# Performance work log

Measured on AMD Instinct MI355X. Metric: run time of the kernel, lower is better.

Reference implementation:

```python
import jax, jax.numpy as jnp
import numpy as np
import math

N_HEAD = 16
K_SPARSE = 64

def setup_inputs() -> dict:
    key = jax.random.key(0)
    ks = jax.random.split(key, 12)
    B, T, C = 1, 2048, 1024
    s = 0.02
    return {
        "x":   jax.random.normal(ks[0], (B, T, C), jnp.float32),
        "Wq":  jax.random.normal(ks[1], (C, C), jnp.float32) * s,
        "bq":  jax.random.normal(ks[2], (C,), jnp.float32) * s,
        "Wk":  jax.random.normal(ks[3], (C, C), jnp.float32) * s,
        "bk":  jax.random.normal(ks[4], (C,), jnp.float32) * s,
        "Wv":  jax.random.normal(ks[5], (C, C), jnp.float32) * s,
        "bv":  jax.random.normal(ks[6], (C,), jnp.float32) * s,
        "Wo":  jax.random.normal(ks[7], (C, C), jnp.float32) * s,
        "bo":  jax.random.normal(ks[8], (C,), jnp.float32) * s,
        "Wks": jax.random.normal(ks[9], (C,), jnp.float32) * s,
        "bks": jax.random.normal(ks[10], (), jnp.float32) * s,
    }

def reference(x, Wq, bq, Wk, bk, Wv, bv, Wo, bo, Wks, bks):
    B, T, C = x.shape
    nh = N_HEAD
    hs = C // nh
    k_val = min(K_SPARSE, T)

    # projections -> (B, nh, T, hs)   (torch Linear: x @ W.T + b)
    q = (x @ Wq.T + bq).reshape(B, T, nh, hs).transpose(0, 2, 1, 3)
    k = (x @ Wk.T + bk).reshape(B, T, nh, hs).transpose(0, 2, 1, 3)
    v = (x @ Wv.T + bv).reshape(B, T, nh, hs).transpose(0, 2, 1, 3)

    # key scorer: per-token scalar score (B, T)
    key_scores = x @ Wks + bks

    # causal masking of scores, then per-query top-k key selection
    pos = jnp.arange(T)
    causal = pos[None, :] <= pos[:, None]                      # (T, T), True where key<=query
    masked = jnp.where(causal[None], key_scores[:, None, :], -jnp.inf)  # (B, T, T)
    _, top_k_idx = jax.lax.top_k(masked, k_val)                # (B, T, k)
    top_k_idx = jnp.minimum(top_k_idx, pos[None, :, None])     # clamp to <= query pos

    # gather sparse keys/values: (B, nh, T, k, hs)
    bi = jnp.arange(B)[:, None, None, None]
    hi = jnp.arange(nh)[None, :, None, None]
    gi = top_k_idx[:, None, :, :]                              # (B, 1, T, k)
    sparse_k = k[bi, hi, gi]                                   # (B, nh, T, k, hs)
    sparse_v = v[bi, hi, gi]

    scale = 1.0 / math.sqrt(hs)
    logits = jnp.einsum('bhtd,bhtkd->bhtk', q, sparse_k) * scale
    probs = jax.nn.softmax(logits, axis=-1)
    out = jnp.einsum('bhtk,bhtkd->bhtd', probs, sparse_v)      # (B, nh, T, hs)
    out = out.transpose(0, 2, 1, 3).reshape(B, T, C)
    return out @ Wo.T + bo
```

## Files before the change

kernel.cpp:

```cpp
#include <hip/hip_runtime.h>
#include <hip/hip_bf16.h>
#include <cstdint>
#include <cstddef>

#define T_DIM 2048
#define C_DIM 1024
#define NH 16
#define HS 64
#define KSP 64

#define GBM 128
#define GBN 64
#define GBK 64
#define GPAD 72

typedef short short8 __attribute__((ext_vector_type(8)));
typedef float f32x4 __attribute__((ext_vector_type(4)));

__device__ __forceinline__ float bfu2f(unsigned short u) {
  unsigned v = ((unsigned)u) << 16;
  return __builtin_bit_cast(float, v);
}
__device__ __forceinline__ unsigned short f2bfu(float f) {
  unsigned u = __builtin_bit_cast(unsigned, f);
  unsigned r = (u + 0x7fffu + ((u >> 16) & 1u)) >> 16;
  return (unsigned short)r;
}
__device__ __forceinline__ float bflo(unsigned u) {
  return __builtin_bit_cast(float, u << 16);
}
__device__ __forceinline__ float bfhi(unsigned u) {
  return __builtin_bit_cast(float, u & 0xffff0000u);
}

__global__ __launch_bounds__(256) void convert_all_kernel(
    const float* __restrict__ x, const float* __restrict__ Wq,
    const float* __restrict__ Wk, const float* __restrict__ Wv,
    const float* __restrict__ Wo,
    unsigned short* __restrict__ xb, unsigned short* __restrict__ Wqb,
    unsigned short* __restrict__ Wkb, unsigned short* __restrict__ Wvb,
    unsigned short* __restrict__ Wob) {
  const int i = blockIdx.x * 256 + threadIdx.x;
  const int NX4 = T_DIM * C_DIM / 4;
  const int NW4 = C_DIM * C_DIM / 4;
  const float* src;
  unsigned short* dst;
  int j = i;
  if (j < NX4) { src = x; dst = xb; }
  else {
    j -= NX4;
    int w = j / NW4;
    j -= w * NW4;
    src = (w == 0) ? Wq : (w == 1) ? Wk : (w == 2) ? Wv : Wo;
    dst = (w == 0) ? Wqb : (w == 1) ? Wkb : (w == 2) ? Wvb : Wob;
  }
  float4 f = reinterpret_cast<const float4*>(src)[j];
  ushort4 o;
  o.x = f2bfu(f.x); o.y = f2bfu(f.y); o.z = f2bfu(f.z); o.w = f2bfu(f.w);
  reinterpret_cast<ushort4*>(dst)[j] = o;
}

__global__ __launch_bounds__(256) void scores_kernel(
    const float* __restrict__ x, const float* __restrict__ Wks,
    const float* __restrict__ bks, float* __restrict__ scores) {
  const int t = blockIdx.x * 4 + (threadIdx.x >> 6);
  const int lane = threadIdx.x & 63;
  const float* xrow = x + (size_t)t * C_DIM;
  float acc = 0.f;
  #pragma unroll 4
  for (int i = lane; i < C_DIM; i += 64)
    acc += xrow[i] * Wks[i];
  #pragma unroll
  for (int o = 32; o; o >>= 1) acc += __shfl_xor(acc, o);
  if (lane == 0) scores[t] = acc + bks[0];
}

__global__ __launch_bounds__(256) void rank_sort_kernel(
    const float* __restrict__ scores, int* __restrict__ sorted_idx) {
  __shared__ float ss[T_DIM];
  const int tid = threadIdx.x;
  for (int j = tid; j < T_DIM; j += 256) ss[j] = scores[j];
  __syncthreads();
  const int w = tid >> 6, lane = tid & 63;
  const int i = blockIdx.x * 4 + w;
  const float si = ss[i];
  int rank = 0;
  #pragma unroll
  for (int step = 0; step < T_DIM / 64; ++step) {
    const int j = step * 64 + lane;
    const float sj = ss[j];
    rank += (int)((sj > si) || (sj == si && j < i));
  }
  #pragma unroll
  for (int o = 32; o; o >>= 1) rank += __shfl_xor(rank, o);
  if (lane == 0) sorted_idx[rank] = i;
}

__global__ __launch_bounds__(256) void select_topk_kernel(
    const int* __restrict__ sorted_idx, int* __restrict__ topk) {
  __shared__ int ss[T_DIM];
  const int tid = threadIdx.x;
  for (int i = tid; i < T_DIM; i += 256) {
    int s = sorted_idx[i];
    ss[i] = (s < 0) ? 0 : (s > T_DIM - 1 ? T_DIM - 1 : s);
  }
  __syncthreads();
  const int t = blockIdx.x * 4 + (tid >> 6);
  const int lane = tid & 63;
  if (t <= 63) {
    topk[(size_t)t * KSP + lane] = (lane < t) ? lane : t;
  } else {
    const unsigned long long lt_mask = (1ull << lane) - 1ull;
    int count = 0;
    for (int chunk = 0; chunk < T_DIM / 64 && count < KSP; ++chunk) {
      int s = ss[chunk * 64 + lane];
      bool ok = (s <= t);
      unsigned long long m = __ballot(ok);
      int pos = count + __popcll(m & lt_mask);
      if (ok && pos < KSP) topk[(size_t)t * KSP + pos] = s;
      count += __popcll(m);
    }
  }
}

__device__ __forceinline__ void gemm_body_128x64(
    const unsigned short* __restrict__ A, const unsigned short* __restrict__ W,
    f32x4 acc[4][2], int bm, int bn, int tid) {
  __shared__ unsigned short As[GBM][GPAD];
  __shared__ unsigned short Ws[GBN][GPAD];
  const int w = tid >> 6, lane = tid & 63;
  const int quad = lane >> 4, r = lane & 15;
  const int wm = (w >> 1) * 64, wn = (w & 1) * 32;
  const int s_row = tid >> 3;
  const int s_ke = (tid & 7) * 8;
  const unsigned short* Abase = A + (size_t)(bm * GBM + s_row) * C_DIM + s_ke;
  const unsigned short* Wbase = W + (size_t)(bn * GBN + s_row) * C_DIM + s_ke;
  for (int kb = 0; kb < C_DIM; kb += GBK) {
    #pragma unroll
    for (int i = 0; i < 4; ++i)
      *reinterpret_cast<short8*>(&As[s_row + 32 * i][s_ke]) =
          *reinterpret_cast<const short8*>(Abase + kb + (size_t)(32 * i) * C_DIM);
    #pragma unroll
    for (int i = 0; i < 2; ++i)
      *reinterpret_cast<short8*>(&Ws[s_row + 32 * i][s_ke]) =
          *reinterpret_cast<const short8*>(Wbase + kb + (size_t)(32 * i) * C_DIM);
    __syncthreads();
    #pragma unroll
    for (int ks = 0; ks < 2; ++ks) {
      short8 af[4], bfr[2];
      #pragma unroll
      for (int mi = 0; mi < 4; ++mi)
        af[mi] = *reinterpret_cast<const short8*>(&As[wm + mi * 16 + r][ks * 32 + quad * 8]);
      #pragma unroll
      for (int ni = 0; ni < 2; ++ni)
        bfr[ni] = *reinterpret_cast<const short8*>(&Ws[wn + ni * 16 + r][ks * 32 + quad * 8]);
      #pragma unroll
      for (int mi = 0; mi < 4; ++mi)
        #pragma unroll
        for (int ni = 0; ni < 2; ++ni)
          acc[mi][ni] = __builtin_amdgcn_mfma_f32_16x16x32_bf16(af[mi], bfr[ni], acc[mi][ni], 0, 0, 0);
    }
    __syncthreads();
  }
}

__global__ __launch_bounds__(256) void gemm_qkv_kernel(
    const unsigned short* __restrict__ A,
    const unsigned short* __restrict__ Wq, const unsigned short* __restrict__ Wk,
    const unsigned short* __restrict__ Wv,
    const float* __restrict__ bq, const float* __restrict__ bk,
    const float* __restrict__ bv,
    unsigned short* __restrict__ qo, unsigned short* __restrict__ ko,
    unsigned short* __restrict__ vo) {
  const int per = (T_DIM / GBM) * (C_DIM / GBN);
  const int which = blockIdx.x / per;
  const int rem = blockIdx.x % per;
  const int bm = rem / (C_DIM / GBN);
  const int bn = rem % (C_DIM / GBN);
  const unsigned short* W = (which == 0) ? Wq : (which == 1) ? Wk : Wv;
  const float* bias = (which == 0) ? bq : (which == 1) ? bk : bv;
  unsigned short* out = (which == 0) ? qo : (which == 1) ? ko : vo;
  const int tid = threadIdx.x;
  f32x4 acc[4][2] = {};
  gemm_body_128x64(A, W, acc, bm, bn, tid);
  const int w = tid >> 6, lane = tid & 63;
  const int quad = lane >> 4, r = lane & 15;
  const int wm = (w >> 1) * 64, wn = (w & 1) * 32;
  #pragma unroll
  for (int mi = 0; mi < 4; ++mi) {
    #pragma unroll
    for (int ni = 0; ni < 2; ++ni) {
      const int col = bn * GBN + wn + ni * 16 + r;
      const float bf = bias[col];
      #pragma unroll
      for (int i = 0; i < 4; ++i) {
        const int row = bm * GBM + wm + mi * 16 + quad * 4 + i;
        out[(size_t)row * C_DIM + col] = f2bfu(acc[mi][ni][i] + bf);
      }
    }
  }
}

__global__ __launch_bounds__(256) void gemm_o_f32_kernel(
    const unsigned short* __restrict__ A, const unsigned short* __restrict__ W,
    const float* __restrict__ bias, float* __restrict__ out) {
  const int tid = threadIdx.x;
  const int bm = blockIdx.x / (C_DIM / GBN);
  const int bn = blockIdx.x % (C_DIM / GBN);
  f32x4 acc[4][2] = {};
  gemm_body_128x64(A, W, acc, bm, bn, tid);
  const int w = tid >> 6, lane = tid & 63;
  const int quad = lane >> 4, r = lane & 15;
  const int wm = (w >> 1) * 64, wn = (w & 1) * 32;
  #pragma unroll
  for (int mi = 0; mi < 4; ++mi) {
    #pragma unroll
    for (int ni = 0; ni < 2; ++ni) {
      const int col = bn * GBN + wn + ni * 16 + r;
      const float bf = bias[col];
      #pragma unroll
      for (int i = 0; i < 4; ++i) {
        const int row = bm * GBM + wm + mi * 16 + quad * 4 + i;
        out[(size_t)row * C_DIM + col] = acc[mi][ni][i] + bf;
      }
    }
  }
}

__global__ __launch_bounds__(256) void attn_kernel(
    const unsigned short* __restrict__ q, const unsigned short* __restrict__ k,
    const unsigned short* __restrict__ v, const int* __restrict__ topk,
    unsigned short* __restrict__ attn_out) {
  __shared__ int off_s[4][KSP];
  const int t = blockIdx.x >> 2;
  const int hg = blockIdx.x & 3;
  const int tid = threadIdx.x;
  const int w = tid >> 6, lane = tid & 63;
  const int h = hg * 4 + w;
  const int c4 = lane & 15;
  const int ksub = lane >> 4;
  {
    int s = topk[(size_t)t * KSP + lane];
    s = (s < 0) ? 0 : (s > t ? t : s);
    off_s[w][lane] = s * C_DIM;
  }
  float4 q4;
  {
    uint2 qraw = *reinterpret_cast<const uint2*>(
        q + (size_t)t * C_DIM + h * HS + 4 * c4);
    q4.x = 0.125f * bflo(qraw.x);
    q4.y = 0.125f * bfhi(qraw.x);
    q4.z = 0.125f * bflo(qraw.y);
    q4.w = 0.125f * bfhi(qraw.y);
  }
  __builtin_amdgcn_wave_barrier();
  const int hbase = h * HS + 4 * c4;
  float l[16];
  int offr[16];
  #pragma unroll
  for (int jj = 0; jj < 16; ++jj) {
    const int offj = off_s[w][4 * jj + ksub];
    offr[jj] = offj;
    uint2 raw = *reinterpret_cast<const uint2*>(k + offj + hbase);
    float pl = q4.x * bflo(raw.x) + q4.y * bfhi(raw.x)
             + q4.z * bflo(raw.y) + q4.w * bfhi(raw.y);
    pl += __shfl_xor(pl, 1);
    pl += __shfl_xor(pl, 2);
    pl += __shfl_xor(pl, 4);
    pl += __shfl_xor(pl, 8);
    l[jj] = pl;
  }
  float m = l[0];
  #pragma unroll
  for (int jj = 1; jj < 16; ++jj) m = fmaxf(m, l[jj]);
  m = fmaxf(m, __shfl_xor(m, 16));
  m = fmaxf(m, __shfl_xor(m, 32));
  float sum = 0.f;
  #pragma unroll
  for (int jj = 0; jj < 16; ++jj) {
    l[jj] = __expf(l[jj] - m);
    sum += l[jj];
  }
  sum += __shfl_xor(sum, 16);
  sum += __shfl_xor(sum, 32);
  const float rs = 1.0f / sum;
  float a0 = 0.f, a1 = 0.f, a2 = 0.f, a3 = 0.f;
  #pragma unroll
  for (int jj = 0; jj < 16; ++jj) {
    uint2 raw = *reinterpret_cast<const uint2*>(v + offr[jj] + hbase);
    const float p = l[jj] * rs;
    a0 += p * bflo(raw.x);
    a1 += p * bfhi(raw.x);
    a2 += p * bflo(raw.y);
    a3 += p * bfhi(raw.y);
  }
  #pragma unroll
  for (int o = 16; o <= 32; o <<= 1) {
    a0 += __shfl_xor(a0, o);
    a1 += __shfl_xor(a1, o);
    a2 += __shfl_xor(a2, o);
    a3 += __shfl_xor(a3, o);
  }
  if (ksub == 0) {
    ushort4 ov;
    ov.x = f2bfu(a0); ov.y = f2bfu(a1); ov.z = f2bfu(a2); ov.w = f2bfu(a3);
    *reinterpret_cast<ushort4*>(attn_out + (size_t)t * C_DIM + h * HS + 4 * c4) = ov;
  }
}

extern "C" void kernel_launch(void* const* d_in, const int* in_sizes, int n_in,
                              void* d_out, int out_size, void* d_ws, size_t ws_size,
                              hipStream_t stream) {
  const float* x   = (const float*)d_in[0];
  const float* Wq  = (const float*)d_in[1];
  const float* bq  = (const float*)d_in[2];
  const float* Wk  = (const float*)d_in[3];
  const float* bk  = (const float*)d_in[4];
  const float* Wv  = (const float*)d_in[5];
  const float* bv  = (const float*)d_in[6];
  const float* Wo  = (const float*)d_in[7];
  const float* bo  = (const float*)d_in[8];
  const float* Wks = (const float*)d_in[9];
  const float* bks = (const float*)d_in[10];
  float* out = (float*)d_out;

  char* ws = (char*)d_ws;
  size_t off = 0;
  float* scores = (float*)(ws + off); off += 8192;
  int*   sorted = (int*)(ws + off);   off += 8192;
  int*   topk   = (int*)(ws + off);   off += (size_t)T_DIM * KSP * 4;
  unsigned short* xb  = (unsigned short*)(ws + off); off += (size_t)T_DIM * C_DIM * 2;
  unsigned short* Wqb = (unsigned short*)(ws + off); off += (size_t)C_DIM * C_DIM * 2;
  unsigned short* Wkb = (unsigned short*)(ws + off); off += (size_t)C_DIM * C_DIM * 2;
  unsigned short* Wvb = (unsigned short*)(ws + off); off += (size_t)C_DIM * C_DIM * 2;
  unsigned short* Wob = (unsigned short*)(ws + off); off += (size_t)C_DIM * C_DIM * 2;
  unsigned short* qb  = (unsigned short*)(ws + off); off += (size_t)T_DIM * C_DIM * 2;
  unsigned short* kb  = (unsigned short*)(ws + off); off += (size_t)T_DIM * C_DIM * 2;
  unsigned short* vb  = (unsigned short*)(ws + off); off += (size_t)T_DIM * C_DIM * 2;
  unsigned short* ab  = xb;

  const int n4_total = (T_DIM * C_DIM + 4 * C_DIM * C_DIM) / 4;
  convert_all_kernel<<<n4_total / 256, 256, 0, stream>>>(
      x, Wq, Wk, Wv, Wo, xb, Wqb, Wkb, Wvb, Wob);

  scores_kernel<<<T_DIM / 4, 256, 0, stream>>>(x, Wks, bks, scores);
  rank_sort_kernel<<<T_DIM / 4, 256, 0, stream>>>(scores, sorted);
  select_topk_kernel<<<T_DIM / 4, 256, 0, stream>>>(sorted, topk);

  gemm_qkv_kernel<<<3 * (T_DIM / GBM) * (C_DIM / GBN), 256, 0, stream>>>(
      xb, Wqb, Wkb, Wvb, bq, bk, bv, qb, kb, vb);

  attn_kernel<<<T_DIM * 4, 256, 0, stream>>>(qb, kb, vb, topk, ab);

  gemm_o_f32_kernel<<<(T_DIM / GBM) * (C_DIM / GBN), 256, 0, stream>>>(
      ab, Wob, bo, out);
}
```

Before: 178.3 us.

## Use direct global-to-LDS loads with XOR swizzle in GEMM; widen attention loads

```diff
diff --git a/kernel.cpp b/kernel.cpp
--- a/kernel.cpp
+++ b/kernel.cpp
@@ -12,7 +12,6 @@
 #define GBM 128
 #define GBN 64
 #define GBK 64
-#define GPAD 72
 
 typedef short short8 __attribute__((ext_vector_type(8)));
 typedef float f32x4 __attribute__((ext_vector_type(4)));
@@ -32,6 +31,11 @@
 __device__ __forceinline__ float bfhi(unsigned u) {
   return __builtin_bit_cast(float, u & 0xffff0000u);
 }
+
+#define GLOAD_LDS16(gp, lp)                                                  \
+  __builtin_amdgcn_global_load_lds(                                          \
+      (const __attribute__((address_space(1))) void*)(gp),                   \
+      (__attribute__((address_space(3))) void*)(lp), 16, 0, 0)
 
 __global__ __launch_bounds__(256) void convert_all_kernel(
     const float* __restrict__ x, const float* __restrict__ Wq,
@@ -126,34 +130,43 @@
 __device__ __forceinline__ void gemm_body_128x64(
     const unsigned short* __restrict__ A, const unsigned short* __restrict__ W,
     f32x4 acc[4][2], int bm, int bn, int tid) {
-  __shared__ unsigned short As[GBM][GPAD];
-  __shared__ unsigned short Ws[GBN][GPAD];
+  __shared__ unsigned short As[GBM * GBK];
+  __shared__ unsigned short Ws[GBN * GBK];
   const int w = tid >> 6, lane = tid & 63;
   const int quad = lane >> 4, r = lane & 15;
   const int wm = (w >> 1) * 64, wn = (w & 1) * 32;
-  const int s_row = tid >> 3;
-  const int s_ke = (tid & 7) * 8;
-  const unsigned short* Abase = A + (size_t)(bm * GBM + s_row) * C_DIM + s_ke;
-  const unsigned short* Wbase = W + (size_t)(bn * GBN + s_row) * C_DIM + s_ke;
+  const int sub = lane >> 3;
+  const int c = lane & 7;
+  const unsigned short* Arow[4];
+  const unsigned short* Wrow[2];
+  #pragma unroll
+  for (int i = 0; i < 4; ++i) {
+    const int row = w * 32 + i * 8 + sub;
+    Arow[i] = A + (size_t)(bm * GBM + row) * C_DIM + ((c ^ (row & 7)) * 8);
+  }
+  #pragma unroll
+  for (int i = 0; i < 2; ++i) {
+    const int row = w * 16 + i * 8 + sub;
+    Wrow[i] = W + (size_t)(bn * GBN + row) * C_DIM + ((c ^ (row & 7)) * 8);
+  }
   for (int kb = 0; kb < C_DIM; kb += GBK) {
     #pragma unroll
     for (int i = 0; i < 4; ++i)
-      *reinterpret_cast<short8*>(&As[s_row + 32 * i][s_ke]) =
-          *reinterpret_cast<const short8*>(Abase + kb + (size_t)(32 * i) * C_DIM);
+      GLOAD_LDS16(Arow[i] + kb, &As[(w * 32 + i * 8) * GBK]);
     #pragma unroll
     for (int i = 0; i < 2; ++i)
-      *reinterpret_cast<short8*>(&Ws[s_row + 32 * i][s_ke]) =
-          *reinterpret_cast<const short8*>(Wbase + kb + (size_t)(32 * i) * C_DIM);
+      GLOAD_LDS16(Wrow[i] + kb, &Ws[(w * 16 + i * 8) * GBK]);
     __syncthreads();
     #pragma unroll
     for (int ks = 0; ks < 2; ++ks) {
+      const int pc = ((ks * 4 + quad) ^ (r & 7)) * 8;
       short8 af[4], bfr[2];
       #pragma unroll
       for (int mi = 0; mi < 4; ++mi)
-        af[mi] = *reinterpret_cast<const short8*>(&As[wm + mi * 16 + r][ks * 32 + quad * 8]);
+        af[mi] = *reinterpret_cast<const short8*>(&As[(wm + mi * 16 + r) * GBK + pc]);
       #pragma unroll
       for (int ni = 0; ni < 2; ++ni)
-        bfr[ni] = *reinterpret_cast<const short8*>(&Ws[wn + ni * 16 + r][ks * 32 + quad * 8]);
+        bfr[ni] = *reinterpret_cast<const short8*>(&Ws[(wn + ni * 16 + r) * GBK + pc]);
       #pragma unroll
       for (int mi = 0; mi < 4; ++mi)
         #pragma unroll
@@ -237,74 +250,77 @@
   const int tid = threadIdx.x;
   const int w = tid >> 6, lane = tid & 63;
   const int h = hg * 4 + w;
-  const int c4 = lane & 15;
-  const int ksub = lane >> 4;
+  const int c8 = lane & 7;
+  const int ksub = lane >> 3;
   {
     int s = topk[(size_t)t * KSP + lane];
     s = (s < 0) ? 0 : (s > t ? t : s);
     off_s[w][lane] = s * C_DIM;
   }
-  float4 q4;
+  const int hbase = h * HS + 8 * c8;
+  float qv[8];
   {
-    uint2 qraw = *reinterpret_cast<const uint2*>(
-        q + (size_t)t * C_DIM + h * HS + 4 * c4);
-    q4.x = 0.125f * bflo(qraw.x);
-    q4.y = 0.125f * bfhi(qraw.x);
-    q4.z = 0.125f * bflo(qraw.y);
-    q4.w = 0.125f * bfhi(qraw.y);
+    uint4 qraw = *reinterpret_cast<const uint4*>(q + (size_t)t * C_DIM + hbase);
+    qv[0] = 0.125f * bflo(qraw.x); qv[1] = 0.125f * bfhi(qraw.x);
+    qv[2] = 0.125f * bflo(qraw.y); qv[3] = 0.125f * bfhi(qraw.y);
+    qv[4] = 0.125f * bflo(qraw.z); qv[5] = 0.125f * bfhi(qraw.z);
+    qv[6] = 0.125f * bflo(qraw.w); qv[7] = 0.125f * bfhi(qraw.w);
   }
   __builtin_amdgcn_wave_barrier();
-  const int hbase = h * HS + 4 * c4;
-  float l[16];
-  int offr[16];
-  #pragma unroll
-  for (int jj = 0; jj < 16; ++jj) {
-    const int offj = off_s[w][4 * jj + ksub];
+  float l[8];
+  int offr[8];
+  #pragma unroll
+  for (int jj = 0; jj < 8; ++jj) {
+    const int offj = off_s[w][8 * jj + ksub];
     offr[jj] = offj;
-    uint2 raw = *reinterpret_cast<const uint2*>(k + offj + hbase);
-    float pl = q4.x * bflo(raw.x) + q4.y * bfhi(raw.x)
-             + q4.z * bflo(raw.y) + q4.w * bfhi(raw.y);
+    uint4 raw = *reinterpret_cast<const uint4*>(k + offj + hbase);
+    float pl = qv[0] * bflo(raw.x) + qv[1] * bfhi(raw.x)
+             + qv[2] * bflo(raw.y) + qv[3] * bfhi(raw.y)
+             + qv[4] * bflo(raw.z) + qv[5] * bfhi(raw.z)
+             + qv[6] * bflo(raw.w) + qv[7] * bfhi(raw.w);
     pl += __shfl_xor(pl, 1);
     pl += __shfl_xor(pl, 2);
     pl += __shfl_xor(pl, 4);
-    pl += __shfl_xor(pl, 8);
     l[jj] = pl;
   }
   float m = l[0];
   #pragma unroll
-  for (int jj = 1; jj < 16; ++jj) m = fmaxf(m, l[jj]);
+  for (int jj = 1; jj < 8; ++jj) m = fmaxf(m, l[jj]);
+  m = fmaxf(m, __shfl_xor(m, 8));
   m = fmaxf(m, __shfl_xor(m, 16));
   m = fmaxf(m, __shfl_xor(m, 32));
   float sum = 0.f;
   #pragma unroll
-  for (int jj = 0; jj < 16; ++jj) {
+  for (int jj = 0; jj < 8; ++jj) {
     l[jj] = __expf(l[jj] - m);
     sum += l[jj];
   }
+  sum += __shfl_xor(sum, 8);
   sum += __shfl_xor(sum, 16);
   sum += __shfl_xor(sum, 32);
   const float rs = 1.0f / sum;
-  float a0 = 0.f, a1 = 0.f, a2 = 0.f, a3 = 0.f;
-  #pragma unroll
-  for (int jj = 0; jj < 16; ++jj) {
-    uint2 raw = *reinterpret_cast<const uint2*>(v + offr[jj] + hbase);
+  float a[8] = {0.f, 0.f, 0.f, 0.f, 0.f, 0.f, 0.f, 0.f};
+  #pragma unroll
+  for (int jj = 0; jj < 8; ++jj) {
+    uint4 raw = *reinterpret_cast<const uint4*>(v + offr[jj] + hbase);
     const float p = l[jj] * rs;
-    a0 += p * bflo(raw.x);
-    a1 += p * bfhi(raw.x);
-    a2 += p * bflo(raw.y);
-    a3 += p * bfhi(raw.y);
-  }
-  #pragma unroll
-  for (int o = 16; o <= 32; o <<= 1) {
-    a0 += __shfl_xor(a0, o);
-    a1 += __shfl_xor(a1, o);
-    a2 += __shfl_xor(a2, o);
-    a3 += __shfl_xor(a3, o);
+    a[0] += p * bflo(raw.x); a[1] += p * bfhi(raw.x);
+    a[2] += p * bflo(raw.y); a[3] += p * bfhi(raw.y);
+    a[4] += p * bflo(raw.z); a[5] += p * bfhi(raw.z);
+    a[6] += p * bflo(raw.w); a[7] += p * bfhi(raw.w);
+  }
+  #pragma unroll
+  for (int o = 8; o <= 32; o <<= 1) {
+    #pragma unroll
+    for (int z = 0; z < 8; ++z) a[z] += __shfl_xor(a[z], o);
   }
   if (ksub == 0) {
-    ushort4 ov;
-    ov.x = f2bfu(a0); ov.y = f2bfu(a1); ov.z = f2bfu(a2); ov.w = f2bfu(a3);
-    *reinterpret_cast<ushort4*>(attn_out + (size_t)t * C_DIM + h * HS + 4 * c4) = ov;
+    ushort4 o0, o1;
+    o0.x = f2bfu(a[0]); o0.y = f2bfu(a[1]); o0.z = f2bfu(a[2]); o0.w = f2bfu(a[3]);
+    o1.x = f2bfu(a[4]); o1.y = f2bfu(a[5]); o1.z = f2bfu(a[6]); o1.w = f2bfu(a[7]);
+    ushort4* dst = reinterpret_cast<ushort4*>(attn_out + (size_t)t * C_DIM + hbase);
+    dst[0] = o0;
+    dst[1] = o1;
   }
 }
 
```

Result: faster. 172.0 us (-3.5%).
